# Optimization experiments

Hardware: AMD Instinct MI355X
Metric: run time of the kernel (lower is better)

## Reference

```python
import jax, jax.numpy as jnp
import numpy as np

EPS = 1e-5

def prelu(x, a):
    return jnp.where(x >= 0, x, a * x)

def batch_norm(x, axes):
    # training-mode BatchNorm with gamma=1, beta=0 (init values)
    m = jnp.mean(x, axis=axes, keepdims=True)
    v = jnp.var(x, axis=axes, keepdims=True)
    return (x - m) / jnp.sqrt(v + EPS)

def conv_branch(X, w, b):
    # X: [B,N,F]; Conv2d(1,1,(1,k)) over the feature axis, VALID
    lhs = X[:, None, :, :]                      # [B,1,N,F]
    rhs = w.reshape(1, 1, 1, -1)                # OIHW
    out = jax.lax.conv_general_dilated(lhs, rhs, (1, 1), 'VALID',
        dimension_numbers=('NCHW', 'OIHW', 'NCHW'))
    return out[:, 0] + b                        # [B,N,F-k+1]

def setup_inputs() -> dict:
    key = jax.random.key(0)
    ks = jax.random.split(key, 16)
    B, N, F, H, D = 8192, 29, 147, 4, 128
    d_cat = 429
    s = 0.05
    return {
        'X': jax.random.normal(ks[0], (B, N, F), jnp.float32),
        'corr': jax.random.uniform(ks[1], (B, N, N), jnp.float32),
        'w_c1': s * jax.random.normal(ks[2], (3,), jnp.float32),
        'b_c1': jnp.zeros((1,), jnp.float32),
        'w_c2': s * jax.random.normal(ks[3], (5,), jnp.float32),
        'b_c2': jnp.zeros((1,), jnp.float32),
        'w_c3': s * jax.random.normal(ks[4], (7,), jnp.float32),
        'b_c3': jnp.zeros((1,), jnp.float32),
        'a_cnn': 0.25 * jnp.ones((1,), jnp.float32),
        'Wg': s * jax.random.normal(ks[5], (d_cat, D), jnp.float32),
        'bg': jnp.zeros((D,), jnp.float32),
        'a_gnn': 0.25 * jnp.ones((1,), jnp.float32),
        'centroids': jax.random.normal(ks[6], (H, 1, D), jnp.float32),
        'head_w': s * jax.random.normal(ks[7], (H,), jnp.float32),
        'Wp': s * jax.random.normal(ks[8], (D, D), jnp.float32),
        'bp': jnp.zeros((D,), jnp.float32),
        'Wm1': s * jax.random.normal(ks[9], (D, D), jnp.float32),
        'bm1': jnp.zeros((D,), jnp.float32),
        'a_mlp': 0.25 * jnp.ones((1,), jnp.float32),
        'Wm2': s * jax.random.normal(ks[10], (D, 1), jnp.float32),
        'bm2': jnp.zeros((1,), jnp.float32),
    }

def reference(X, corr, w_c1, b_c1, w_c2, b_c2, w_c3, b_c3, a_cnn,
              Wg, bg, a_gnn, centroids, head_w, Wp, bp,
              Wm1, bm1, a_mlp, Wm2, bm2):
    # three conv branches + concat + PReLU + BN over node channels
    a1 = conv_branch(X, w_c1, b_c1)             # [B,29,145]
    a2 = conv_branch(X, w_c2, b_c2)             # [B,29,143]
    a3 = conv_branch(X, w_c3, b_c3)             # [B,29,141]
    x = prelu(jnp.concatenate([a1, a2, a3], axis=2), a_cnn)  # [B,29,429]
    x = batch_norm(x, (0, 2))
    # GraphConv: A x W + b
    x = jnp.einsum('bnm,bmd->bnd', corr, x) @ Wg + bg        # [B,29,128]
    x = prelu(x, a_gnn)
    x = batch_norm(x, (0, 2))
    # CoSimPool: multi-head cosine-sim attention assignment to 1 cluster
    xn = x / (jnp.linalg.norm(x, axis=-1, keepdims=True) + 1e-8)
    cn = centroids / (jnp.linalg.norm(centroids, axis=-1, keepdims=True) + 1e-8)
    sim = jnp.einsum('hmd,bnd->bhmn', cn, xn)                # [B,4,1,29]
    agg = jnp.einsum('h,bhmn->bmn', head_w, sim)             # 1x1 conv over heads
    C = jax.nn.softmax(agg, axis=-1)                         # [B,1,29]
    x = jnp.einsum('bmn,bnd->bmd', C, x) @ Wp + bp           # [B,1,128]
    x = x[:, 0]                                              # squeeze(1)
    x = batch_norm(x, (0,))
    h = prelu(x @ Wm1 + bm1, a_mlp)
    y = jax.nn.sigmoid(h @ Wm2 + bm2)                        # [B,1]
    return y
```

## Files before the change

kernel.cpp:

```cpp
#include <hip/hip_runtime.h>

#define B_    8192
#define N_    29
#define F_    147
#define DC    429
#define D_    128
#define ROWS  (B_*N_)
#define EPSBN 1e-5f

#define UTSTR   4096
#define RS_SH   3712

#define X3_OFF   16777216
#define ACC_OFF  (X3_OFF + B_*D_)
#define BN1_OFF  (ACC_OFF)
#define BN2_OFF  (ACC_OFF + 1856)
#define BN3_OFF  (ACC_OFF + 3712)
#define FIN_OFF  (ACC_OFF + 11904)
#define CSW_OFF  (FIN_OFF + 384)
#define V_OFF    (FIN_OFF + 512)
#define V1_OFF   (FIN_OFF + 640)
#define CSWP_OFF (FIN_OFF + 768)
#define IMG_OFF  (FIN_OFF + 1024)
#define WPI_OFF  (IMG_OFF + 28672)
#define WM1I_OFF (WPI_OFF + 8192)

typedef __bf16 bf16x8 __attribute__((ext_vector_type(8)));
typedef float  f32x4  __attribute__((ext_vector_type(4)));

__device__ __forceinline__ unsigned short f2bf(float f) {
  unsigned int u = __float_as_uint(f);
  u += 0x7fffu + ((u >> 16) & 1u);
  return (unsigned short)(u >> 16);
}
__device__ __forceinline__ float bf2f(unsigned u16) {
  return __uint_as_float(u16 << 16);
}

#define TSTR 456
#define UTILS 34
#define ATSTR 136

__global__ void k0a_img(const float* __restrict__ Wg, const float* __restrict__ Wp,
                        const float* __restrict__ Wm1, float* __restrict__ ws)
{
  const int tid = threadIdx.x;
  if (blockIdx.x < 16) {
    __shared__ float cs_l[8];
    const int kb = blockIdx.x * 8;
    if (tid < 8) cs_l[tid] = 0.f;
    __syncthreads();
    unsigned short* img = (unsigned short*)(ws + IMG_OFF);
    for (int i = tid; i < 8*448; i += 256) {
      int kk = i / 448, dk = i - kk*448;
      int k = kb + kk;
      int d;
      if      (dk < 145)  d = dk;
      else if (dk == 145) d = -1;
      else if (dk < 289)  d = dk - 1;
      else if (dk == 289) d = -1;
      else if (dk < 431)  d = dk - 2;
      else                d = -1;
      float v = (d >= 0) ? Wg[(size_t)d*D_ + k] : 0.f;
      img[(size_t)k*448 + dk] = f2bf(v);
      if (d >= 0) atomicAdd(&cs_l[kk], v);
    }
    __syncthreads();
    if (tid < 8) ws[CSW_OFF + kb + tid] = cs_l[tid];
  } else if (blockIdx.x == 16) {
    unsigned short* wpi = (unsigned short*)(ws + WPI_OFF);
    for (int i = tid; i < 16384; i += 256) {
      int k = i >> 7, c = i & 127;
      wpi[c*128 + k] = f2bf(Wp[k*128 + c]);
    }
    if (tid < 128) {
      float s = 0.f;
      for (int k = 0; k < 128; ++k) s += Wp[k*128 + tid];
      ws[CSWP_OFF + tid] = s;
    }
  } else {
    unsigned short* wmi = (unsigned short*)(ws + WM1I_OFF);
    for (int i = tid; i < 16384; i += 256) {
      int k = i >> 7, c = i & 127;
      wmi[c*128 + k] = f2bf(Wm1[k*128 + c]);
    }
  }
}

__global__ void k0b_cent(const float* __restrict__ cent, const float* __restrict__ hw,
                         float* __restrict__ ws)
{
  __shared__ float sq[128];
  __shared__ float nrm;
  const int tid = threadIdx.x;
  float vk = 0.f;
  for (int h = 0; h < 4; ++h) {
    float c = cent[h*D_ + tid];
    sq[tid] = c*c;
    __syncthreads();
    if (tid == 0) { float s=0.f; for (int j=0;j<128;++j) s+=sq[j]; nrm = sqrtf(s)+1e-8f; }
    __syncthreads();
    vk += hw[h] * c / nrm;
    __syncthreads();
  }
  ws[V_OFF + tid] = vk;
  sq[tid] = vk;
  __syncthreads();
  if (tid == 0) { float s=0.f; for (int j=0;j<128;++j) s+=sq[j]; ws[V1_OFF] = s; }
}

__global__ __launch_bounds__(512, 2) void k1_conv_gemm(
    const float* __restrict__ X,
    const float* __restrict__ wc1, const float* __restrict__ bc1,
    const float* __restrict__ wc2, const float* __restrict__ bc2,
    const float* __restrict__ wc3, const float* __restrict__ bc3,
    const float* __restrict__ acnn, float* __restrict__ ws)
{
  __shared__ __align__(16) unsigned short t_s[64*TSTR];
  const int tid = threadIdx.x;
  const int b0 = blockIdx.x * 2;

  {
    float* xs = (float*)t_s;
    const float* Xb = X + (size_t)b0 * (N_ * F_);
    for (int i = tid; i < 58*147; i += 512) {
      int rr = i / 147;
      int cc = i - rr*147;
      xs[rr*148 + cc] = Xb[i];
    }
  }
  __syncthreads();

  const float c10 = wc1[0], c11 = wc1[1], c12 = wc1[2], b1 = bc1[0];
  const float c20 = wc2[0], c21 = wc2[1], c22 = wc2[2], c23 = wc2[3], c24 = wc2[4], b2 = bc2[0];
  const float c30 = wc3[0], c31 = wc3[1], c32 = wc3[2], c33 = wc3[3], c34 = wc3[4],
              c35 = wc3[5], c36 = wc3[6], b3 = bc3[0];
  const float ap = acnn[0];

  const int rC = tid >> 3, qC = tid & 7;
  const int bbC = rC >> 5, nC = rC & 31;
  const bool act = (nC < 29);
  const int f0 = qC * 19;
  const int nld = act ? nC : 28;
  float xv[25];
  {
    const float* xrow = (const float*)t_s + (bbC*29 + nld)*148 + f0;
    #pragma unroll
    for (int i = 0; i < 25; ++i) xv[i] = xrow[i];
  }
  __syncthreads();

  for (int i = tid; i < 2*3*448; i += 512) {
    int bbz = i / (3*448), rem = i - bbz*(3*448);
    int r = rem / 448, c = rem - r*448;
    t_s[(bbz*32 + 29 + r)*TSTR + c] = 0;
  }
  for (int i = tid; i < 58*19; i += 512) {
    int rr = i / 19, j = i - rr*19;
    int bbz = (rr >= 29), n = rr - bbz*29;
    int col = (j == 0) ? 145 : ((j == 1) ? 289 : (429 + j));
    t_s[(bbz*32 + n)*TSTR + col] = 0;
  }

  {
    float s1 = 0.f, s2 = 0.f;
    unsigned short* tr = t_s + (bbC*32 + nC)*TSTR;
    if (act) {
      if (qC < 7) {
        #pragma unroll
        for (int i = 0; i < 19; ++i) {
          float v1 = fmaf(xv[i],c10, fmaf(xv[i+1],c11, fmaf(xv[i+2],c12, b1)));
          v1 = (v1 >= 0.f) ? v1 : ap*v1;
          s1 += v1; s2 = fmaf(v1, v1, s2);
          tr[f0 + i] = f2bf(v1);
          float v2 = fmaf(xv[i],c20, fmaf(xv[i+1],c21, fmaf(xv[i+2],c22, fmaf(xv[i+3],c23, fmaf(xv[i+4],c24, b2)))));
          v2 = (v2 >= 0.f) ? v2 : ap*v2;
          s1 += v2; s2 = fmaf(v2, v2, s2);
          tr[146 + f0 + i] = f2bf(v2);
          float v3 = fmaf(xv[i],c30, fmaf(xv[i+1],c31, fmaf(xv[i+2],c32, fmaf(xv[i+3],c33, fmaf(xv[i+4],c34, fmaf(xv[i+5],c35, fmaf(xv[i+6],c36, b3)))))));
          v3 = (v3 >= 0.f) ? v3 : ap*v3;
          s1 += v3; s2 = fmaf(v3, v3, s2);
          tr[290 + f0 + i] = f2bf(v3);
        }
      } else {
        #pragma unroll
        for (int i = 0; i < 12; ++i) {
          float v1 = fmaf(xv[i],c10, fmaf(xv[i+1],c11, fmaf(xv[i+2],c12, b1)));
          v1 = (v1 >= 0.f) ? v1 : ap*v1;
          s1 += v1; s2 = fmaf(v1, v1, s2);
          tr[133 + i] = f2bf(v1);
        }
        #pragma unroll
        for (int i = 0; i < 10; ++i) {
          float v2 = fmaf(xv[i],c20, fmaf(xv[i+1],c21, fmaf(xv[i+2],c22, fmaf(xv[i+3],c23, fmaf(xv[i+4],c24, b2)))));
          v2 = (v2 >= 0.f) ? v2 : ap*v2;
          s1 += v2; s2 = fmaf(v2, v2, s2);
          tr[279 + i] = f2bf(v2);
        }
        #pragma unroll
        for (int i = 0; i < 8; ++i) {
          float v3 = fmaf(xv[i],c30, fmaf(xv[i+1],c31, fmaf(xv[i+2],c32, fmaf(xv[i+3],c33, fmaf(xv[i+4],c34, fmaf(xv[i+5],c35, fmaf(xv[i+6],c36, b3)))))));
          v3 = (v3 >= 0.f) ? v3 : ap*v3;
          s1 += v3; s2 = fmaf(v3, v3, s2);
          tr[423 + i] = f2bf(v3);
        }
      }
    }
    #pragma unroll
    for (int off = 4; off >= 1; off >>= 1) {
      s1 += __shfl_xor(s1, off);
      s2 += __shfl_xor(s2, off);
    }
    if (act && qC == 0) {
      float* bn1 = ws + BN1_OFF + (size_t)(blockIdx.x & 31) * 58;
      atomicAdd(&bn1[nC*2+0], s1);
      atomicAdd(&bn1[nC*2+1], s2);
    }
  }
  __syncthreads();

  const int wv = tid >> 6, lane = tid & 63;
  const int lrow = lane & 15, quad = lane >> 4;
  const int bb = wv >> 2;
  const int n0 = (wv & 3) * 32;
  const unsigned short* imgp = (const unsigned short*)(ws + IMG_OFF);
  const unsigned short* gB0 = imgp + (size_t)(n0 + lrow)*448 + quad*8;
  const unsigned short* gB1 = gB0 + 16*448;
  const unsigned short* tA = t_s + (size_t)(bb*32)*TSTR + quad*8;

  f32x4 a00 = (f32x4){0.f,0.f,0.f,0.f}, a01 = a00, a10 = a00, a11 = a00;
  bf16x8 Bc0 = *(const bf16x8*)(gB0);
  bf16x8 Bc1 = *(const bf16x8*)(gB1);
  #pragma unroll
  for (int ks = 0; ks < 14; ++ks) {
    bf16x8 Bn0, Bn1;
    if (ks < 13) {
      Bn0 = *(const bf16x8*)(gB0 + (ks+1)*32);
      Bn1 = *(const bf16x8*)(gB1 + (ks+1)*32);
    }
    bf16x8 A0 = *(const bf16x8*)(tA + lrow*TSTR + ks*32);
    bf16x8 A1 = *(const bf16x8*)(tA + (16+lrow)*TSTR + ks*32);
    a00 = __builtin_amdgcn_mfma_f32_16x16x32_bf16(A0, Bc0, a00, 0, 0, 0);
    a01 = __builtin_amdgcn_mfma_f32_16x16x32_bf16(A0, Bc1, a01, 0, 0, 0);
    a10 = __builtin_amdgcn_mfma_f32_16x16x32_bf16(A1, Bc0, a10, 0, 0, 0);
    a11 = __builtin_amdgcn_mfma_f32_16x16x32_bf16(A1, Bc1, a11, 0, 0, 0);
    Bc0 = Bn0; Bc1 = Bn1;
  }
  __syncthreads();

  {
    unsigned short* ut = t_s + bb*4352;
    const int fb0 = n0 + lrow, fb1 = n0 + 16 + lrow;
    #pragma unroll
    for (int i = 0; i < 4; ++i) {
      int m0 = quad*4 + i, m1 = 16 + quad*4 + i;
      ut[fb0*UTILS + m0] = f2bf(a00[i]);
      ut[fb1*UTILS + m0] = f2bf(a01[i]);
      ut[fb0*UTILS + m1] = f2bf(a10[i]);
      ut[fb1*UTILS + m1] = f2bf(a11[i]);
    }
  }
  __syncthreads();
  {
    const unsigned* u32t = (const unsigned*)t_s;
    unsigned short* ws16 = (unsigned short*)ws;
    #pragma unroll
    for (int it = 0; it < 8; ++it) {
      int idx = tid + it*512;
      int bbs = idx >> 11, rem = idx & 2047;
      int f = rem >> 4, pr = rem & 15;
      unsigned* Ug = (unsigned*)(ws16 + (size_t)(b0 + bbs)*UTSTR);
      Ug[f*16 + pr] = u32t[bbs*2176 + f*17 + pr];
    }
  }
}

__global__ __launch_bounds__(256) void k3_gnn(
    const float* __restrict__ corr, const float* __restrict__ bg,
    const float* __restrict__ agnn, float* __restrict__ ws)
{
  __shared__ float cwf[841];
  __shared__ unsigned short a_s[32*40];
  __shared__ float m1s[29], is1s[29], cms[29], st1s[29], st2s[29], svs[29];

  const int b = blockIdx.x, tid = threadIdx.x;
  const int wv = tid >> 6, lane = tid & 63;
  const int lrow = lane & 15, quad = lane >> 4;
  unsigned short* Utb = (unsigned short*)ws + (size_t)b * UTSTR;

  if (tid < 29) {
    float s1 = 0.f, s2 = 0.f;
    #pragma unroll 4
    for (int s = 0; s < 32; ++s) {
      s1 += ws[BN1_OFF + s*58 + tid*2 + 0];
      s2 += ws[BN1_OFF + s*58 + tid*2 + 1];
    }
    const float inv = 1.f / (float)(B_ * DC);
    float mean = s1 * inv;
    float var  = s2 * inv - mean * mean;
    m1s[tid] = mean; is1s[tid] = rsqrtf(var + EPSBN);
    st1s[tid] = 0.f; st2s[tid] = 0.f; svs[tid] = 0.f;
  }
  const float* cb = corr + (size_t)b * 841;
  for (int i = tid; i < 841; i += 256) cwf[i] = cb[i];
  __syncthreads();

  const int f0 = wv * 32;
  bf16x8 B0 = *(const bf16x8*)&Utb[(f0      + lrow)*32 + quad*8];
  bf16x8 B1 = *(const bf16x8*)&Utb[(f0 + 16 + lrow)*32 + quad*8];

  for (int i = tid; i < 1024; i += 256) {
    int n = i >> 5, m = i & 31;
    float v = (n < 29 && m < 29) ? cwf[n*29 + m] * is1s[m] : 0.f;
    a_s[n*40 + m] = f2bf(v);
  }
  if (tid < 29) {
    float cm = 0.f;
    for (int m = 0; m < 29; ++m) cm = fmaf(cwf[tid*29 + m] * is1s[m], m1s[m], cm);
    cms[tid] = cm;
  }
  __syncthreads();

  bf16x8 A0 = *(const bf16x8*)&a_s[lrow*40 + quad*8];
  bf16x8 A1 = *(const bf16x8*)&a_s[(16 + lrow)*40 + quad*8];
  f32x4 acc[2][2];
  acc[0][0] = (f32x4){0.f,0.f,0.f,0.f}; acc[0][1] = (f32x4){0.f,0.f,0.f,0.f};
  acc[1][0] = (f32x4){0.f,0.f,0.f,0.f}; acc[1][1] = (f32x4){0.f,0.f,0.f,0.f};
  acc[0][0] = __builtin_amdgcn_mfma_f32_16x16x32_bf16(A0, B0, acc[0][0], 0, 0, 0);
  acc[0][1] = __builtin_amdgcn_mfma_f32_16x16x32_bf16(A0, B1, acc[0][1], 0, 0, 0);
  acc[1][0] = __builtin_amdgcn_mfma_f32_16x16x32_bf16(A1, B0, acc[1][0], 0, 0, 0);
  acc[1][1] = __builtin_amdgcn_mfma_f32_16x16x32_bf16(A1, B1, acc[1][1], 0, 0, 0);
  __syncthreads();

  const float ag = agnn[0];
  const float vA  = ws[V_OFF  + f0 + lrow],      vB  = ws[V_OFF  + f0 + 16 + lrow];
  const float csA = ws[CSW_OFF + f0 + lrow],     csB = ws[CSW_OFF + f0 + 16 + lrow];
  const float bgA = bg[f0 + lrow],               bgB = bg[f0 + 16 + lrow];
  #pragma unroll
  for (int mt = 0; mt < 2; ++mt) {
    #pragma unroll
    for (int i = 0; i < 4; ++i) {
      int n = mt*16 + quad*4 + i;
      if (n < 29) {
        float y0 = acc[mt][0][i] - cms[n]*csA + bgA;
        float y1 = acc[mt][1][i] - cms[n]*csB + bgB;
        y0 = (y0 >= 0.f) ? y0 : ag*y0;
        y1 = (y1 >= 0.f) ? y1 : ag*y1;
        Utb[n*D_ + f0 + lrow]      = f2bf(y0);
        Utb[n*D_ + f0 + 16 + lrow] = f2bf(y1);
        float sy  = y0 + y1;
        float sy2 = fmaf(y0, y0, y1*y1);
        float sv  = fmaf(y0, vA, y1*vB);
        #pragma unroll
        for (int off = 8; off >= 1; off >>= 1) {
          sy  += __shfl_xor(sy, off);
          sy2 += __shfl_xor(sy2, off);
          sv  += __shfl_xor(sv, off);
        }
        if (lrow == 0) {
          atomicAdd(&st1s[n], sy);
          atomicAdd(&st2s[n], sy2);
          atomicAdd(&svs[n],  sv);
        }
      }
    }
  }
  __syncthreads();
  if (tid < 29) {
    float* rs = (float*)(Utb + RS_SH);
    rs[tid]      = st1s[tid];
    rs[29 + tid] = st2s[tid];
    rs[58 + tid] = svs[tid];
    float* bn2 = ws + BN2_OFF + (size_t)(b & 31) * 58;
    atomicAdd(&bn2[tid*2+0], st1s[tid]);
    atomicAdd(&bn2[tid*2+1], st2s[tid]);
  }
}

__global__ __launch_bounds__(256) void k4_pool(
    const float* __restrict__ bpv, float* __restrict__ ws)
{
  __shared__ unsigned short Atile[32*ATSTR];
  __shared__ float m2s[29], is2s[29], koffs[32];
  const int tid = threadIdx.x, wv = tid >> 6, lane = tid & 63;
  const int b0 = blockIdx.x * 32;
  const unsigned short* U16 = (const unsigned short*)ws;

  if (tid < 29) {
    float s1 = 0.f, s2 = 0.f;
    #pragma unroll 4
    for (int s = 0; s < 32; ++s) {
      s1 += ws[BN2_OFF + s*58 + tid*2 + 0];
      s2 += ws[BN2_OFF + s*58 + tid*2 + 1];
    }
    const float inv = 1.f / (float)(B_ * D_);
    float mean = s1 * inv, var = s2 * inv - mean * mean;
    m2s[tid] = mean; is2s[tid] = rsqrtf(var + EPSBN);
  }
  __syncthreads();

  const float V1 = ws[V1_OFF];
  unsigned* At32 = (unsigned*)Atile;
  for (int mb = 0; mb < 8; ++mb) {
    const int m = wv*8 + mb;
    const unsigned short* yb = U16 + (size_t)(b0 + m) * UTSTR;
    const float* rs = (const float*)(yb + RS_SH);
    float agg = -1e30f, m2 = 0.f, is2 = 0.f;
    if (lane < 29) {
      float S1 = rs[lane], S2 = rs[29+lane], Sv = rs[58+lane];
      m2 = m2s[lane]; is2 = is2s[lane];
      float ss = fmaxf(S2 - 2.f*m2*S1 + 128.f*m2*m2, 0.f);
      agg = (is2*(Sv - m2*V1)) / (is2*sqrtf(ss) + 1e-8f);
    }
    float mx = agg;
    #pragma unroll
    for (int off = 32; off >= 1; off >>= 1) mx = fmaxf(mx, __shfl_xor(mx, off));
    float e = (lane < 29) ? __expf(agg - mx) : 0.f;
    float den = e, kof = e*is2*m2;
    #pragma unroll
    for (int off = 32; off >= 1; off >>= 1) { den += __shfl_xor(den, off); kof += __shfl_xor(kof, off); }
    float rden = 1.f / den;
    float c = e * is2 * rden;
    if (lane == 0) koffs[m] = kof * rden;
    const unsigned* y32 = (const unsigned*)yb;
    float p0 = 0.f, p1 = 0.f;
    #pragma unroll
    for (int n = 0; n < 29; ++n) {
      float cn = __shfl(c, n);
      unsigned u = y32[n*64 + lane];
      p0 = fmaf(cn, bf2f(u & 0xffffu), p0);
      p1 = fmaf(cn, bf2f(u >> 16), p1);
    }
    At32[m*68 + lane] = (unsigned)f2bf(p0) | ((unsigned)f2bf(p1) << 16);
  }
  __syncthreads();

  const int lrow = lane & 15, quad = lane >> 4;
  const int n0 = wv * 32;
  const unsigned short* wpi = (const unsigned short*)(ws + WPI_OFF);
  f32x4 acc[2][2];
  acc[0][0] = (f32x4){0.f,0.f,0.f,0.f}; acc[0][1] = acc[0][0];
  acc[1][0] = acc[0][0]; acc[1][1] = acc[0][0];
  #pragma unroll
  for (int ks = 0; ks < 4; ++ks) {
    bf16x8 A0 = *(const bf16x8*)&Atile[lrow*ATSTR + ks*32 + quad*8];
    bf16x8 A1 = *(const bf16x8*)&Atile[(16+lrow)*ATSTR + ks*32 + quad*8];
    bf16x8 Bq0 = *(const bf16x8*)&wpi[(size_t)(n0 + lrow)*128 + ks*32 + quad*8];
    bf16x8 Bq1 = *(const bf16x8*)&wpi[(size_t)(n0 + 16 + lrow)*128 + ks*32 + quad*8];
    acc[0][0] = __builtin_amdgcn_mfma_f32_16x16x32_bf16(A0, Bq0, acc[0][0], 0, 0, 0);
    acc[0][1] = __builtin_amdgcn_mfma_f32_16x16x32_bf16(A0, Bq1, acc[0][1], 0, 0, 0);
    acc[1][0] = __builtin_amdgcn_mfma_f32_16x16x32_bf16(A1, Bq0, acc[1][0], 0, 0, 0);
    acc[1][1] = __builtin_amdgcn_mfma_f32_16x16x32_bf16(A1, Bq1, acc[1][1], 0, 0, 0);
  }

  float* bn3 = ws + BN3_OFF + (size_t)(blockIdx.x & 31) * 256;
  #pragma unroll
  for (int nt = 0; nt < 2; ++nt) {
    int col = n0 + nt*16 + lrow;
    float cswp = ws[CSWP_OFF + col], bp = bpv[col];
    float s1c = 0.f, s2c = 0.f;
    #pragma unroll
    for (int mt = 0; mt < 2; ++mt) {
      #pragma unroll
      for (int i = 0; i < 4; ++i) {
        int m = mt*16 + quad*4 + i;
        float x3 = acc[mt][nt][i] - koffs[m]*cswp + bp;
        ws[X3_OFF + (size_t)(b0 + m)*D_ + col] = x3;
        s1c += x3; s2c = fmaf(x3, x3, s2c);
      }
    }
    s1c += __shfl_xor(s1c, 16); s1c += __shfl_xor(s1c, 32);
    s2c += __shfl_xor(s2c, 16); s2c += __shfl_xor(s2c, 32);
    if (quad == 0) {
      atomicAdd(&bn3[col*2+0], s1c);
      atomicAdd(&bn3[col*2+1], s2c);
    }
  }
}

__global__ __launch_bounds__(256) void k5_mlp(
    const float* __restrict__ bm1, const float* __restrict__ amlp,
    const float* __restrict__ Wm2, const float* __restrict__ bm2,
    float* __restrict__ ws, float* __restrict__ out)
{
  __shared__ unsigned short Atile[32*ATSTR];
  __shared__ float m3s[128], is3s[128], logit_s[32];
  const int tid = threadIdx.x, wv = tid >> 6, lane = tid & 63;
  const int b0 = blockIdx.x * 32;

  if (tid < 128) {
    float s1 = 0.f, s2 = 0.f;
    #pragma unroll 4
    for (int s = 0; s < 32; ++s) {
      s1 += ws[BN3_OFF + s*256 + tid*2 + 0];
      s2 += ws[BN3_OFF + s*256 + tid*2 + 1];
    }
    const float inv = 1.f / (float)B_;
    float mean = s1 * inv, var = s2 * inv - mean * mean;
    m3s[tid] = mean; is3s[tid] = rsqrtf(var + EPSBN);
  }
  if (tid >= 128 && tid < 160) logit_s[tid-128] = 0.f;
  __syncthreads();

  for (int it = 0; it < 16; ++it) {
    int idx = tid + it*256;
    int row = idx >> 7, col = idx & 127;
    float v = (ws[X3_OFF + (size_t)(b0+row)*D_ + col] - m3s[col]) * is3s[col];
    Atile[row*ATSTR + col] = f2bf(v);
  }
  __syncthreads();

  const int lrow = lane & 15, quad = lane >> 4;
  const int n0 = wv * 32;
  const unsigned short* wmi = (const unsigned short*)(ws + WM1I_OFF);
  f32x4 acc[2][2];
  acc[0][0] = (f32x4){0.f,0.f,0.f,0.f}; acc[0][1] = acc[0][0];
  acc[1][0] = acc[0][0]; acc[1][1] = acc[0][0];
  #pragma unroll
  for (int ks = 0; ks < 4; ++ks) {
    bf16x8 A0 = *(const bf16x8*)&Atile[lrow*ATSTR + ks*32 + quad*8];
    bf16x8 A1 = *(const bf16x8*)&Atile[(16+lrow)*ATSTR + ks*32 + quad*8];
    bf16x8 Bq0 = *(const bf16x8*)&wmi[(size_t)(n0 + lrow)*128 + ks*32 + quad*8];
    bf16x8 Bq1 = *(const bf16x8*)&wmi[(size_t)(n0 + 16 + lrow)*128 + ks*32 + quad*8];
    acc[0][0] = __builtin_amdgcn_mfma_f32_16x16x32_bf16(A0, Bq0, acc[0][0], 0, 0, 0);
    acc[0][1] = __builtin_amdgcn_mfma_f32_16x16x32_bf16(A0, Bq1, acc[0][1], 0, 0, 0);
    acc[1][0] = __builtin_amdgcn_mfma_f32_16x16x32_bf16(A1, Bq0, acc[1][0], 0, 0, 0);
    acc[1][1] = __builtin_amdgcn_mfma_f32_16x16x32_bf16(A1, Bq1, acc[1][1], 0, 0, 0);
  }

  const float am = amlp[0];
  float bmc[2], wm2c[2];
  #pragma unroll
  for (int nt = 0; nt < 2; ++nt) {
    int col = n0 + nt*16 + lrow;
    bmc[nt] = bm1[col]; wm2c[nt] = Wm2[col];
  }
  #pragma unroll
  for (int mt = 0; mt < 2; ++mt) {
    #pragma unroll
    for (int i = 0; i < 4; ++i) {
      float pm = 0.f;
      #pragma unroll
      for (int nt = 0; nt < 2; ++nt) {
        float h = acc[mt][nt][i] + bmc[nt];
        h = (h >= 0.f) ? h : am*h;
        pm = fmaf(h, wm2c[nt], pm);
      }
      #pragma unroll
      for (int off = 8; off >= 1; off >>= 1) pm += __shfl_xor(pm, off);
      if (lrow == 0) atomicAdd(&logit_s[mt*16 + quad*4 + i], pm);
    }
  }
  __syncthreads();
  if (tid < 32) {
    float logit = logit_s[tid] + bm2[0];
    out[b0 + tid] = 1.f / (1.f + expf(-logit));
  }
}

extern "C" void kernel_launch(void* const* d_in, const int* in_sizes, int n_in,
                              void* d_out, int out_size, void* d_ws, size_t ws_size,
                              hipStream_t stream)
{
  (void)in_sizes; (void)n_in; (void)out_size; (void)ws_size;
  const float* X    = (const float*)d_in[0];
  const float* corr = (const float*)d_in[1];
  const float* wc1  = (const float*)d_in[2];
  const float* bc1  = (const float*)d_in[3];
  const float* wc2  = (const float*)d_in[4];
  const float* bc2  = (const float*)d_in[5];
  const float* wc3  = (const float*)d_in[6];
  const float* bc3  = (const float*)d_in[7];
  const float* acnn = (const float*)d_in[8];
  const float* Wg   = (const float*)d_in[9];
  const float* bg   = (const float*)d_in[10];
  const float* agnn = (const float*)d_in[11];
  const float* cent = (const float*)d_in[12];
  const float* hw   = (const float*)d_in[13];
  const float* Wp   = (const float*)d_in[14];
  const float* bp   = (const float*)d_in[15];
  const float* Wm1  = (const float*)d_in[16];
  const float* bm1  = (const float*)d_in[17];
  const float* amlp = (const float*)d_in[18];
  const float* Wm2  = (const float*)d_in[19];
  const float* bm2  = (const float*)d_in[20];
  float* ws  = (float*)d_ws;
  float* out = (float*)d_out;

  hipMemsetAsync(ws + ACC_OFF, 0, 11904 * sizeof(float), stream);
  k0a_img<<<18, 256, 0, stream>>>(Wg, Wp, Wm1, ws);
  k0b_cent<<<1, 128, 0, stream>>>(cent, hw, ws);
  k1_conv_gemm<<<B_/2, 512, 0, stream>>>(X, wc1, bc1, wc2, bc2, wc3, bc3, acnn, ws);
  k3_gnn<<<B_, 256, 0, stream>>>(corr, bg, agnn, ws);
  k4_pool<<<B_/32, 256, 0, stream>>>(bp, ws);
  k5_mlp<<<B_/32, 256, 0, stream>>>(bm1, amlp, Wm2, bm2, ws, out);
}
```

Before: 479.0 us.

## Split conv-gemm to one batch per block, hoist BN1 finalize, deepen B prefetch

The conv+GEMM kernel now processes one batch element per 256-thread block instead of two per 512-thread block, halving shared memory per block to raise occupancy. The BN1 statistics reduction is moved out of every k3_gnn block into a tiny separate kernel, so each gnn block only reads the precomputed mean and inverse std. The B-operand prefetch becomes double-buffered two steps ahead. The cms dot product switches to a wave shuffle reduction, and bf16 conversion uses the native cast. Together these add one kernel launch and change the rounding path for the bf16 conversion.

After: 465.2 us. 1.03x faster.

```diff
diff --git a/kernel.cpp b/kernel.cpp
--- a/kernel.cpp
+++ b/kernel.cpp
@@ -29,9 +29,8 @@
 typedef float  f32x4  __attribute__((ext_vector_type(4)));
 
 __device__ __forceinline__ unsigned short f2bf(float f) {
-  unsigned int u = __float_as_uint(f);
-  u += 0x7fffu + ((u >> 16) & 1u);
-  return (unsigned short)(u >> 16);
+  __bf16 h = (__bf16)f;
+  return __builtin_bit_cast(unsigned short, h);
 }
 __device__ __forceinline__ float bf2f(unsigned u16) {
   return __uint_as_float(u16 << 16);
@@ -109,21 +108,21 @@
   if (tid == 0) { float s=0.f; for (int j=0;j<128;++j) s+=sq[j]; ws[V1_OFF] = s; }
 }
 
-__global__ __launch_bounds__(512, 2) void k1_conv_gemm(
+__global__ __launch_bounds__(256, 5) void k1_conv_gemm(
     const float* __restrict__ X,
     const float* __restrict__ wc1, const float* __restrict__ bc1,
     const float* __restrict__ wc2, const float* __restrict__ bc2,
     const float* __restrict__ wc3, const float* __restrict__ bc3,
     const float* __restrict__ acnn, float* __restrict__ ws)
 {
-  __shared__ __align__(16) unsigned short t_s[64*TSTR];
+  __shared__ __align__(16) unsigned short t_s[32*TSTR];
   const int tid = threadIdx.x;
-  const int b0 = blockIdx.x * 2;
+  const int b = blockIdx.x;
 
   {
     float* xs = (float*)t_s;
-    const float* Xb = X + (size_t)b0 * (N_ * F_);
-    for (int i = tid; i < 58*147; i += 512) {
+    const float* Xb = X + (size_t)b * (N_ * F_);
+    for (int i = tid; i < 29*147; i += 256) {
       int rr = i / 147;
       int cc = i - rr*147;
       xs[rr*148 + cc] = Xb[i];
@@ -137,34 +136,31 @@
               c35 = wc3[5], c36 = wc3[6], b3 = bc3[0];
   const float ap = acnn[0];
 
-  const int rC = tid >> 3, qC = tid & 7;
-  const int bbC = rC >> 5, nC = rC & 31;
+  const int nC = tid >> 3, qC = tid & 7;
   const bool act = (nC < 29);
   const int f0 = qC * 19;
   const int nld = act ? nC : 28;
   float xv[25];
   {
-    const float* xrow = (const float*)t_s + (bbC*29 + nld)*148 + f0;
+    const float* xrow = (const float*)t_s + nld*148 + f0;
     #pragma unroll
     for (int i = 0; i < 25; ++i) xv[i] = xrow[i];
   }
   __syncthreads();
 
-  for (int i = tid; i < 2*3*448; i += 512) {
-    int bbz = i / (3*448), rem = i - bbz*(3*448);
-    int r = rem / 448, c = rem - r*448;
-    t_s[(bbz*32 + 29 + r)*TSTR + c] = 0;
-  }
-  for (int i = tid; i < 58*19; i += 512) {
-    int rr = i / 19, j = i - rr*19;
-    int bbz = (rr >= 29), n = rr - bbz*29;
+  for (int i = tid; i < 3*448; i += 256) {
+    int r = i / 448, c = i - r*448;
+    t_s[(29 + r)*TSTR + c] = 0;
+  }
+  for (int i = tid; i < 29*19; i += 256) {
+    int n = i / 19, j = i - n*19;
     int col = (j == 0) ? 145 : ((j == 1) ? 289 : (429 + j));
-    t_s[(bbz*32 + n)*TSTR + col] = 0;
+    t_s[n*TSTR + col] = 0;
   }
 
   {
     float s1 = 0.f, s2 = 0.f;
-    unsigned short* tr = t_s + (bbC*32 + nC)*TSTR;
+    unsigned short* tr = t_s + nC*TSTR;
     if (act) {
       if (qC < 7) {
         #pragma unroll
@@ -221,22 +217,24 @@
 
   const int wv = tid >> 6, lane = tid & 63;
   const int lrow = lane & 15, quad = lane >> 4;
-  const int bb = wv >> 2;
-  const int n0 = (wv & 3) * 32;
+  const int n0 = wv * 32;
   const unsigned short* imgp = (const unsigned short*)(ws + IMG_OFF);
   const unsigned short* gB0 = imgp + (size_t)(n0 + lrow)*448 + quad*8;
   const unsigned short* gB1 = gB0 + 16*448;
-  const unsigned short* tA = t_s + (size_t)(bb*32)*TSTR + quad*8;
+  const unsigned short* tA = t_s + quad*8;
 
   f32x4 a00 = (f32x4){0.f,0.f,0.f,0.f}, a01 = a00, a10 = a00, a11 = a00;
-  bf16x8 Bc0 = *(const bf16x8*)(gB0);
-  bf16x8 Bc1 = *(const bf16x8*)(gB1);
+  bf16x8 Br0[2], Br1[2];
+  Br0[0] = *(const bf16x8*)(gB0);
+  Br1[0] = *(const bf16x8*)(gB1);
+  Br0[1] = *(const bf16x8*)(gB0 + 32);
+  Br1[1] = *(const bf16x8*)(gB1 + 32);
   #pragma unroll
   for (int ks = 0; ks < 14; ++ks) {
-    bf16x8 Bn0, Bn1;
-    if (ks < 13) {
-      Bn0 = *(const bf16x8*)(gB0 + (ks+1)*32);
-      Bn1 = *(const bf16x8*)(gB1 + (ks+1)*32);
+    bf16x8 Bc0 = Br0[ks & 1], Bc1 = Br1[ks & 1];
+    if (ks < 12) {
+      Br0[ks & 1] = *(const bf16x8*)(gB0 + (ks+2)*32);
+      Br1[ks & 1] = *(const bf16x8*)(gB1 + (ks+2)*32);
     }
     bf16x8 A0 = *(const bf16x8*)(tA + lrow*TSTR + ks*32);
     bf16x8 A1 = *(const bf16x8*)(tA + (16+lrow)*TSTR + ks*32);
@@ -244,12 +242,11 @@
     a01 = __builtin_amdgcn_mfma_f32_16x16x32_bf16(A0, Bc1, a01, 0, 0, 0);
     a10 = __builtin_amdgcn_mfma_f32_16x16x32_bf16(A1, Bc0, a10, 0, 0, 0);
     a11 = __builtin_amdgcn_mfma_f32_16x16x32_bf16(A1, Bc1, a11, 0, 0, 0);
-    Bc0 = Bn0; Bc1 = Bn1;
   }
   __syncthreads();
 
   {
-    unsigned short* ut = t_s + bb*4352;
+    unsigned short* ut = t_s;
     const int fb0 = n0 + lrow, fb1 = n0 + 16 + lrow;
     #pragma unroll
     for (int i = 0; i < 4; ++i) {
@@ -264,14 +261,31 @@
   {
     const unsigned* u32t = (const unsigned*)t_s;
     unsigned short* ws16 = (unsigned short*)ws;
+    unsigned* Ug = (unsigned*)(ws16 + (size_t)b * UTSTR);
     #pragma unroll
     for (int it = 0; it < 8; ++it) {
-      int idx = tid + it*512;
-      int bbs = idx >> 11, rem = idx & 2047;
-      int f = rem >> 4, pr = rem & 15;
-      unsigned* Ug = (unsigned*)(ws16 + (size_t)(b0 + bbs)*UTSTR);
-      Ug[f*16 + pr] = u32t[bbs*2176 + f*17 + pr];
-    }
+      int idx = tid + it*256;
+      int f = idx >> 4, pr = idx & 15;
+      Ug[f*16 + pr] = u32t[f*17 + pr];
+    }
+  }
+}
+
+__global__ void k2_bn1f(float* __restrict__ ws)
+{
+  const int n = threadIdx.x;
+  if (n < 29) {
+    float s1 = 0.f, s2 = 0.f;
+    #pragma unroll 4
+    for (int s = 0; s < 32; ++s) {
+      s1 += ws[BN1_OFF + s*58 + n*2 + 0];
+      s2 += ws[BN1_OFF + s*58 + n*2 + 1];
+    }
+    const float inv = 1.f / (float)(B_ * DC);
+    float mean = s1 * inv;
+    float var  = s2 * inv - mean * mean;
+    ws[FIN_OFF + n]      = mean;
+    ws[FIN_OFF + 32 + n] = rsqrtf(var + EPSBN);
   }
 }
 
@@ -281,43 +295,37 @@
 {
   __shared__ float cwf[841];
   __shared__ unsigned short a_s[32*40];
-  __shared__ float m1s[29], is1s[29], cms[29], st1s[29], st2s[29], svs[29];
+  __shared__ float m1s[29], is1s[29], cms[32], st1s[29], st2s[29], svs[29];
 
   const int b = blockIdx.x, tid = threadIdx.x;
   const int wv = tid >> 6, lane = tid & 63;
   const int lrow = lane & 15, quad = lane >> 4;
   unsigned short* Utb = (unsigned short*)ws + (size_t)b * UTSTR;
 
-  if (tid < 29) {
-    float s1 = 0.f, s2 = 0.f;
-    #pragma unroll 4
-    for (int s = 0; s < 32; ++s) {
-      s1 += ws[BN1_OFF + s*58 + tid*2 + 0];
-      s2 += ws[BN1_OFF + s*58 + tid*2 + 1];
-    }
-    const float inv = 1.f / (float)(B_ * DC);
-    float mean = s1 * inv;
-    float var  = s2 * inv - mean * mean;
-    m1s[tid] = mean; is1s[tid] = rsqrtf(var + EPSBN);
-    st1s[tid] = 0.f; st2s[tid] = 0.f; svs[tid] = 0.f;
-  }
-  const float* cb = corr + (size_t)b * 841;
-  for (int i = tid; i < 841; i += 256) cwf[i] = cb[i];
-  __syncthreads();
-
   const int f0 = wv * 32;
   bf16x8 B0 = *(const bf16x8*)&Utb[(f0      + lrow)*32 + quad*8];
   bf16x8 B1 = *(const bf16x8*)&Utb[(f0 + 16 + lrow)*32 + quad*8];
 
-  for (int i = tid; i < 1024; i += 256) {
+  if (tid < 29) {
+    m1s[tid]  = ws[FIN_OFF + tid];
+    is1s[tid] = ws[FIN_OFF + 32 + tid];
+    st1s[tid] = 0.f; st2s[tid] = 0.f; svs[tid] = 0.f;
+  }
+  const float* cb = corr + (size_t)b * 841;
+  for (int i = tid; i < 841; i += 256) cwf[i] = cb[i];
+  __syncthreads();
+
+  #pragma unroll
+  for (int it = 0; it < 4; ++it) {
+    int i = tid + it*256;
     int n = i >> 5, m = i & 31;
-    float v = (n < 29 && m < 29) ? cwf[n*29 + m] * is1s[m] : 0.f;
+    bool val = (n < 29 && m < 29);
+    float v = val ? cwf[n*29 + m] * is1s[m] : 0.f;
     a_s[n*40 + m] = f2bf(v);
-  }
-  if (tid < 29) {
-    float cm = 0.f;
-    for (int m = 0; m < 29; ++m) cm = fmaf(cwf[tid*29 + m] * is1s[m], m1s[m], cm);
-    cms[tid] = cm;
+    float p = val ? v * m1s[m] : 0.f;
+    #pragma unroll
+    for (int off = 16; off >= 1; off >>= 1) p += __shfl_xor(p, off);
+    if (m == 0 && n < 29) cms[n] = p;
   }
   __syncthreads();
 
@@ -590,7 +598,8 @@
   hipMemsetAsync(ws + ACC_OFF, 0, 11904 * sizeof(float), stream);
   k0a_img<<<18, 256, 0, stream>>>(Wg, Wp, Wm1, ws);
   k0b_cent<<<1, 128, 0, stream>>>(cent, hw, ws);
-  k1_conv_gemm<<<B_/2, 512, 0, stream>>>(X, wc1, bc1, wc2, bc2, wc3, bc3, acnn, ws);
+  k1_conv_gemm<<<B_, 256, 0, stream>>>(X, wc1, bc1, wc2, bc2, wc3, bc3, acnn, ws);
+  k2_bn1f<<<1, 64, 0, stream>>>(ws);
   k3_gnn<<<B_, 256, 0, stream>>>(corr, bg, agnn, ws);
   k4_pool<<<B_/32, 256, 0, stream>>>(bp, ws);
   k5_mlp<<<B_/32, 256, 0, stream>>>(bm1, amlp, Wm2, bm2, ws, out);
```
